# Performance work log

Measured on AMD Instinct MI355X. Metric: run time of the kernel, lower is better.

## Reference

```python
import jax, jax.numpy as jnp
import numpy as np

N = 100000      # nodes
DIN = 64        # input feature dim
H = 64          # hidden dim
OUT = 2         # classifier output dim
E_REL = 1600000 # edges per relation
E_Q = 1000000   # query edges to classify


def _deg_norm(idx, n, dtype):
    # D^{-1/2} with zero-degree -> 0 (DGL norm='both' semantics)
    deg = jax.ops.segment_sum(jnp.ones(idx.shape[0], dtype=dtype), idx, num_segments=n)
    return jnp.where(deg > 0, jax.lax.rsqrt(jnp.maximum(deg, 1.0)), 0.0)


def graph_conv(x, src, dst, W, b):
    # DGL GraphConv, norm='both': out = D_in^{-1/2} A D_out^{-1/2} x W + b
    n = x.shape[0]
    c_src = _deg_norm(src, n, x.dtype)   # out-degree norm on src side
    c_dst = _deg_norm(dst, n, x.dtype)   # in-degree norm on dst side
    h = x * c_src[:, None]
    agg = jax.ops.segment_sum(h[src], dst, num_segments=n)  # gather -> scatter-add
    agg = agg * c_dst[:, None]
    return agg @ W + b


def setup_inputs() -> dict:
    key = jax.random.key(0)
    ks = jax.random.split(key, 16)
    x = jax.random.normal(ks[0], (N, DIN), dtype=jnp.float32)
    src_pos = jax.random.randint(ks[1], (E_REL,), 0, N)
    dst_pos = jax.random.randint(ks[2], (E_REL,), 0, N)
    src_neg = jax.random.randint(ks[3], (E_REL,), 0, N)
    dst_neg = jax.random.randint(ks[4], (E_REL,), 0, N)
    edge_index = jax.random.randint(ks[5], (2, E_Q), 0, N)
    s_in = 1.0 / np.sqrt(DIN)
    s_h = 1.0 / np.sqrt(H)
    return {
        "x": x,
        "W0_pos": jax.random.uniform(ks[6], (DIN, H), jnp.float32, -s_in, s_in),
        "b0_pos": jnp.zeros((H,), jnp.float32),
        "W0_neg": jax.random.uniform(ks[7], (DIN, H), jnp.float32, -s_in, s_in),
        "b0_neg": jnp.zeros((H,), jnp.float32),
        "W1_pos": jax.random.uniform(ks[8], (H, H), jnp.float32, -s_h, s_h),
        "b1_pos": jnp.zeros((H,), jnp.float32),
        "W1_neg": jax.random.uniform(ks[9], (H, H), jnp.float32, -s_h, s_h),
        "b1_neg": jnp.zeros((H,), jnp.float32),
        "Wc": jax.random.uniform(ks[10], (2 * H, OUT), jnp.float32, -s_h, s_h),
        "bc": jnp.zeros((OUT,), jnp.float32),
        "src_pos": src_pos, "dst_pos": dst_pos,
        "src_neg": src_neg, "dst_neg": dst_neg,
        "edge_index": edge_index,
    }


def reference(x, W0_pos, b0_pos, W0_neg, b0_neg, W1_pos, b1_pos, W1_neg, b1_neg,
              Wc, bc, src_pos, dst_pos, src_neg, dst_neg, edge_index):
    # Layer 1: per-relation GraphConv on input feats, ReLU (HeteroGraphConv 'all' keeps per-relation streams)
    h_pos = jax.nn.relu(graph_conv(x, src_pos, dst_pos, W0_pos, b0_pos))
    h_neg = jax.nn.relu(graph_conv(x, src_neg, dst_neg, W0_neg, b0_neg))
    # Layer 2: each relation stream convolved on its own relation graph
    z_pos = jax.nn.relu(graph_conv(h_pos, src_pos, dst_pos, W1_pos, b1_pos))
    z_neg = jax.nn.relu(graph_conv(h_neg, src_neg, dst_neg, W1_neg, b1_neg))
    z = z_pos - z_neg                         # [N, H]
    src_ids, dst_ids = edge_index[0], edge_index[1]
    h_pair = jnp.concatenate([z[src_ids], z[dst_ids]], axis=1)  # [E_Q, 2H]
    logits = h_pair @ Wc + bc
    return z, jax.nn.sigmoid(logits)
```

## Files before the change

kernel.cpp:

```cpp
#include <hip/hip_runtime.h>
#include <hip/hip_fp16.h>
#include <math.h>

#define N_NODES 100000
#define DIM 64
#define E_REL 1600000
#define E_QQ 1000000

#define NBUCK 196
#define BCAP 9216
#define CHUNK_E 8192
#define P1_BLOCKS ((E_REL + CHUNK_E - 1) / CHUNK_E)

__global__ __launch_bounds__(256) void bin_edges(
    const int* __restrict__ src, const int* __restrict__ dst,
    int* __restrict__ gcur_d, int* __restrict__ gcur_s,
    unsigned* __restrict__ bin_d, unsigned* __restrict__ bin_s) {
  __shared__ int cd[NBUCK];
  __shared__ int cs[NBUCK];
  int t = threadIdx.x;
  for (int i = t; i < NBUCK; i += 256) { cd[i] = 0; cs[i] = 0; }
  __syncthreads();
  int e0 = blockIdx.x * CHUNK_E;
  int e1 = e0 + CHUNK_E;
  if (e1 > E_REL) e1 = E_REL;
  for (int e = e0 + t; e < e1; e += 256) {
    atomicAdd(&cd[dst[e] >> 9], 1);
    atomicAdd(&cs[src[e] >> 9], 1);
  }
  __syncthreads();
  for (int i = t; i < NBUCK; i += 256) {
    cd[i] = atomicAdd(&gcur_d[i], cd[i]);
    cs[i] = atomicAdd(&gcur_s[i], cs[i]);
  }
  __syncthreads();
  for (int e = e0 + t; e < e1; e += 256) {
    int s = src[e];
    int d = dst[e];
    int bd = d >> 9;
    int bs = s >> 9;
    int pd = atomicAdd(&cd[bd], 1);
    int ps = atomicAdd(&cs[bs], 1);
    if ((unsigned)pd < BCAP)
      bin_d[(size_t)bd * BCAP + pd] = (unsigned)(((d & 511) << 17) | s);
    if ((unsigned)ps < BCAP)
      bin_s[(size_t)bs * BCAP + ps] = (unsigned)s;
  }
}

__global__ __launch_bounds__(256) void build_tables(
    const unsigned* __restrict__ bin_d, const int* __restrict__ gcur_d,
    const unsigned* __restrict__ bin_s, const int* __restrict__ gcur_s,
    int* __restrict__ offs, int* __restrict__ degv, int* __restrict__ srclist,
    float* __restrict__ csrc) {
  __shared__ int cnt[512];
  __shared__ int off0[512];
  __shared__ int curv[512];
  __shared__ int ls[256];
  int t = threadIdx.x;
  if (blockIdx.x >= NBUCK) {
    int b = blockIdx.x - NBUCK;
    cnt[t] = 0;
    cnt[t + 256] = 0;
    __syncthreads();
    int n = gcur_s[b];
    if (n > BCAP) n = BCAP;
    const unsigned* be = bin_s + (size_t)b * BCAP;
    for (int i = t; i < n; i += 256) atomicAdd(&cnt[be[i] & 511], 1);
    __syncthreads();
    int node0 = b << 9;
    for (int i = t; i < 512; i += 256) {
      int node = node0 + i;
      if (node < N_NODES) {
        int d = cnt[i];
        csrc[node] = d > 0 ? rsqrtf((float)d) : 0.0f;
      }
    }
    return;
  }
  int b = blockIdx.x;
  cnt[t] = 0;
  cnt[t + 256] = 0;
  __syncthreads();
  int n = gcur_d[b];
  if (n > BCAP) n = BCAP;
  const unsigned* be = bin_d + (size_t)b * BCAP;
  for (int i = t; i < n; i += 256) atomicAdd(&cnt[be[i] >> 17], 1);
  __syncthreads();
  int c0 = cnt[2 * t], c1 = cnt[2 * t + 1];
  ls[t] = c0 + c1;
  __syncthreads();
  for (int off = 1; off < 256; off <<= 1) {
    int v = (t >= off) ? ls[t - off] : 0;
    __syncthreads();
    ls[t] += v;
    __syncthreads();
  }
  int base = ls[t] - (c0 + c1);
  off0[2 * t] = base;
  off0[2 * t + 1] = base + c0;
  curv[2 * t] = base;
  curv[2 * t + 1] = base + c0;
  __syncthreads();
  for (int i = t; i < n; i += 256) {
    unsigned p = be[i];
    int dl = p >> 17;
    int pos = atomicAdd(&curv[dl], 1);
    srclist[(size_t)b * BCAP + pos] = (int)(p & 0x1FFFF);
  }
  __syncthreads();
  int node0 = b << 9;
  for (int i = t; i < 512; i += 256) {
    int node = node0 + i;
    if (node < N_NODES) {
      offs[node] = b * BCAP + off0[i];
      degv[node] = cnt[i];
    }
  }
}

__device__ inline unsigned pack_h2(float a, float b) {
  __half2 h = __floats2half2_rn(a, b);
  return *reinterpret_cast<unsigned*>(&h);
}

__global__ __launch_bounds__(256) void gemm_in_h(
    const float* __restrict__ X, const float* __restrict__ W,
    const float* __restrict__ csrc, __half* __restrict__ Y) {
  __shared__ float Ws[64 * 64];
  for (int t = threadIdx.x; t < 64 * 64; t += 256) Ws[t] = W[t];
  __syncthreads();
  int row = blockIdx.x * 256 + threadIdx.x;
  if (row >= N_NODES) return;
  const float4* xr = (const float4*)(X + (size_t)row * 64);
  float acc[64];
#pragma unroll
  for (int j = 0; j < 64; j++) acc[j] = 0.0f;
#pragma unroll
  for (int k4 = 0; k4 < 16; k4++) {
    float4 xv = xr[k4];
    const float* w0 = &Ws[(k4 * 4 + 0) * 64];
    const float* w1 = &Ws[(k4 * 4 + 1) * 64];
    const float* w2 = &Ws[(k4 * 4 + 2) * 64];
    const float* w3 = &Ws[(k4 * 4 + 3) * 64];
#pragma unroll
    for (int j = 0; j < 64; j++)
      acc[j] += xv.x * w0[j] + xv.y * w1[j] + xv.z * w2[j] + xv.w * w3[j];
  }
  float s = csrc[row];
  uint4* yr = (uint4*)(Y + (size_t)row * 64);
#pragma unroll
  for (int j8 = 0; j8 < 8; j8++) {
    uint4 u;
    u.x = pack_h2(s * acc[j8 * 8 + 0], s * acc[j8 * 8 + 1]);
    u.y = pack_h2(s * acc[j8 * 8 + 2], s * acc[j8 * 8 + 3]);
    u.z = pack_h2(s * acc[j8 * 8 + 4], s * acc[j8 * 8 + 5]);
    u.w = pack_h2(s * acc[j8 * 8 + 6], s * acc[j8 * 8 + 7]);
    yr[j8] = u;
  }
}

__device__ inline float4 agg_quad(const __half* __restrict__ Y, int beg,
                                  int deg, const int* __restrict__ srclist,
                                  int lane, int l, int q) {
  float4 a0 = make_float4(0.f, 0.f, 0.f, 0.f);
  float4 a1 = make_float4(0.f, 0.f, 0.f, 0.f);
  const __half* Yl = Y + 4 * l;
  for (int base = 0; base < deg; base += 64) {
    int chunk = deg - base;
    if (chunk > 64) chunk = 64;
    int sv = (base + lane < deg) ? srclist[beg + base + lane] : 0;
    int nq8 = chunk & ~7;
    for (int j = 0; j < nq8; j += 8) {
      int s0 = __shfl(sv, j + q);
      int s1 = __shfl(sv, j + 4 + q);
      uint2 u0 = *(const uint2*)(Yl + (size_t)s0 * 64);
      uint2 u1 = *(const uint2*)(Yl + (size_t)s1 * 64);
      float2 f;
      f = __half22float2(*reinterpret_cast<__half2*>(&u0.x));
      a0.x += f.x; a0.y += f.y;
      f = __half22float2(*reinterpret_cast<__half2*>(&u0.y));
      a0.z += f.x; a0.w += f.y;
      f = __half22float2(*reinterpret_cast<__half2*>(&u1.x));
      a1.x += f.x; a1.y += f.y;
      f = __half22float2(*reinterpret_cast<__half2*>(&u1.y));
      a1.z += f.x; a1.w += f.y;
    }
    int j0 = nq8 + q;
    int j1 = nq8 + 4 + q;
    int s0 = __shfl(sv, j0 & 63);
    int s1 = __shfl(sv, j1 & 63);
    if (j0 < chunk) {
      uint2 u = *(const uint2*)(Yl + (size_t)s0 * 64);
      float2 f;
      f = __half22float2(*reinterpret_cast<__half2*>(&u.x));
      a0.x += f.x; a0.y += f.y;
      f = __half22float2(*reinterpret_cast<__half2*>(&u.y));
      a0.z += f.x; a0.w += f.y;
    }
    if (j1 < chunk) {
      uint2 u = *(const uint2*)(Yl + (size_t)s1 * 64);
      float2 f;
      f = __half22float2(*reinterpret_cast<__half2*>(&u.x));
      a1.x += f.x; a1.y += f.y;
      f = __half22float2(*reinterpret_cast<__half2*>(&u.y));
      a1.z += f.x; a1.w += f.y;
    }
  }
  a0.x += a1.x; a0.y += a1.y; a0.z += a1.z; a0.w += a1.w;
  a0.x += __shfl_xor(a0.x, 16); a0.y += __shfl_xor(a0.y, 16);
  a0.z += __shfl_xor(a0.z, 16); a0.w += __shfl_xor(a0.w, 16);
  a0.x += __shfl_xor(a0.x, 32); a0.y += __shfl_xor(a0.y, 32);
  a0.z += __shfl_xor(a0.z, 32); a0.w += __shfl_xor(a0.w, 32);
  return a0;
}

__global__ __launch_bounds__(256) void gather_mid(
    const __half* __restrict__ Y, const int* __restrict__ offs,
    const int* __restrict__ degv, const int* __restrict__ srclist,
    const float* __restrict__ b0, const float* __restrict__ csrc,
    const float* __restrict__ W1, __half* __restrict__ Y2) {
  __shared__ float Ws[64 * 64];
  __shared__ float hs[4][64];
  for (int t = threadIdx.x; t < 64 * 64; t += 256) Ws[t] = W1[t];
  __syncthreads();
  int wid = (blockIdx.x * 256 + threadIdx.x) >> 6;
  int lane = threadIdx.x & 63;
  int wslot = threadIdx.x >> 6;
  if (wid >= N_NODES) return;
  int l = lane & 15, q = lane >> 4;
  int beg = offs[wid];
  int deg = degv[wid];
  float4 acc = agg_quad(Y, beg, deg, srclist, lane, l, q);
  float cd = deg > 0 ? rsqrtf((float)deg) : 0.0f;
  float4 bv = ((const float4*)b0)[l];
  float4 h;
  h.x = fmaxf(acc.x * cd + bv.x, 0.0f);
  h.y = fmaxf(acc.y * cd + bv.y, 0.0f);
  h.z = fmaxf(acc.z * cd + bv.z, 0.0f);
  h.w = fmaxf(acc.w * cd + bv.w, 0.0f);
  if (lane < 16) *((float4*)&hs[wslot][4 * l]) = h;
  float acc2 = 0.0f;
#pragma unroll
  for (int k4 = 0; k4 < 16; k4++) {
    float4 hv = *((const float4*)&hs[wslot][4 * k4]);
    acc2 += hv.x * Ws[(4 * k4 + 0) * 64 + lane] +
            hv.y * Ws[(4 * k4 + 1) * 64 + lane] +
            hv.z * Ws[(4 * k4 + 2) * 64 + lane] +
            hv.w * Ws[(4 * k4 + 3) * 64 + lane];
  }
  Y2[(size_t)wid * 64 + lane] = __float2half(csrc[wid] * acc2);
}

template <int MODE>
__global__ __launch_bounds__(256) void gather_fin(
    const __half* __restrict__ Y2, const int* __restrict__ offs,
    const int* __restrict__ degv, const int* __restrict__ srclist,
    const float* __restrict__ b1, float* __restrict__ z,
    float* __restrict__ uv, const float* __restrict__ Wc) {
  __shared__ float Wcs[256];
  if (MODE == 1) {
    Wcs[threadIdx.x] = Wc[threadIdx.x];
    __syncthreads();
  }
  int wid = (blockIdx.x * 256 + threadIdx.x) >> 6;
  int lane = threadIdx.x & 63;
  if (wid >= N_NODES) return;
  int l = lane & 15, q = lane >> 4;
  int beg = offs[wid];
  int deg = degv[wid];
  float4 acc = agg_quad(Y2, beg, deg, srclist, lane, l, q);
  float cd = deg > 0 ? rsqrtf((float)deg) : 0.0f;
  float4 bv = ((const float4*)b1)[l];
  float4 v;
  v.x = fmaxf(acc.x * cd + bv.x, 0.0f);
  v.y = fmaxf(acc.y * cd + bv.y, 0.0f);
  v.z = fmaxf(acc.z * cd + bv.z, 0.0f);
  v.w = fmaxf(acc.w * cd + bv.w, 0.0f);
  float* zrow = z + (size_t)wid * 64 + 4 * l;
  if (MODE == 0) {
    if (lane < 16) *((float4*)zrow) = v;
  } else {
    float4 zo = *((const float4*)zrow);
    float4 r;
    r.x = zo.x - v.x; r.y = zo.y - v.y; r.z = zo.z - v.z; r.w = zo.w - v.w;
    if (lane < 16) *((float4*)zrow) = r;
    float pu0 = r.x * Wcs[(4 * l + 0) * 2 + 0] + r.y * Wcs[(4 * l + 1) * 2 + 0] +
                r.z * Wcs[(4 * l + 2) * 2 + 0] + r.w * Wcs[(4 * l + 3) * 2 + 0];
    float pu1 = r.x * Wcs[(4 * l + 0) * 2 + 1] + r.y * Wcs[(4 * l + 1) * 2 + 1] +
                r.z * Wcs[(4 * l + 2) * 2 + 1] + r.w * Wcs[(4 * l + 3) * 2 + 1];
    float pv0 = r.x * Wcs[(64 + 4 * l + 0) * 2 + 0] + r.y * Wcs[(64 + 4 * l + 1) * 2 + 0] +
                r.z * Wcs[(64 + 4 * l + 2) * 2 + 0] + r.w * Wcs[(64 + 4 * l + 3) * 2 + 0];
    float pv1 = r.x * Wcs[(64 + 4 * l + 0) * 2 + 1] + r.y * Wcs[(64 + 4 * l + 1) * 2 + 1] +
                r.z * Wcs[(64 + 4 * l + 2) * 2 + 1] + r.w * Wcs[(64 + 4 * l + 3) * 2 + 1];
#pragma unroll
    for (int o = 1; o < 16; o <<= 1) {
      pu0 += __shfl_xor(pu0, o);
      pu1 += __shfl_xor(pu1, o);
      pv0 += __shfl_xor(pv0, o);
      pv1 += __shfl_xor(pv1, o);
    }
    if (lane == 0) {
      float4 o4 = make_float4(pu0, pu1, pv0, pv1);
      *((float4*)(uv + (size_t)wid * 4)) = o4;
    }
  }
}

__global__ __launch_bounds__(256) void classify_kernel(
    const float* __restrict__ uv, const int* __restrict__ ei,
    const float* __restrict__ bc, float* __restrict__ out) {
  int e = blockIdx.x * 256 + threadIdx.x;
  if (e >= E_QQ) return;
  int s = ei[e];
  int d = ei[E_QQ + e];
  float4 us = *((const float4*)(uv + (size_t)s * 4));
  float4 vd = *((const float4*)(uv + (size_t)d * 4));
  float l0 = us.x + vd.z + bc[0];
  float l1 = us.y + vd.w + bc[1];
  float2 o;
  o.x = 1.0f / (1.0f + __expf(-l0));
  o.y = 1.0f / (1.0f + __expf(-l1));
  *((float2*)(out + (size_t)e * 2)) = o;
}

extern "C" void kernel_launch(void* const* d_in, const int* in_sizes, int n_in,
                              void* d_out, int out_size, void* d_ws,
                              size_t ws_size, hipStream_t stream) {
  const float* x   = (const float*)d_in[0];
  const float* W0p = (const float*)d_in[1];
  const float* b0p = (const float*)d_in[2];
  const float* W0n = (const float*)d_in[3];
  const float* b0n = (const float*)d_in[4];
  const float* W1p = (const float*)d_in[5];
  const float* b1p = (const float*)d_in[6];
  const float* W1n = (const float*)d_in[7];
  const float* b1n = (const float*)d_in[8];
  const float* Wc  = (const float*)d_in[9];
  const float* bc  = (const float*)d_in[10];
  const int* sp = (const int*)d_in[11];
  const int* dp = (const int*)d_in[12];
  const int* sn = (const int*)d_in[13];
  const int* dn = (const int*)d_in[14];
  const int* ei = (const int*)d_in[15];

  float* csrc_p = (float*)d_ws;
  float* csrc_n = csrc_p + N_NODES;
  int* offs_p = (int*)(csrc_n + N_NODES);
  int* deg_p  = offs_p + N_NODES;
  int* offs_n = deg_p + N_NODES;
  int* deg_n  = offs_n + N_NODES;
  float* uv   = (float*)(deg_n + N_NODES);
  int* gcur   = (int*)(uv + 4 * N_NODES);
  unsigned* bin_d = (unsigned*)(gcur + 2 * NBUCK + 2);
  unsigned* bin_s = bin_d + (size_t)NBUCK * BCAP;
  int* srclist = (int*)(bin_s + (size_t)NBUCK * BCAP);
  __half* A = (__half*)(srclist + (size_t)NBUCK * BCAP);
  __half* B = A + (size_t)N_NODES * 64;

  float* z     = (float*)d_out;
  float* probs = z + (size_t)N_NODES * 64;

  int* gcur_d = gcur;
  int* gcur_s = gcur + NBUCK;

  const int gemmGrid = (N_NODES + 255) / 256;
  const int aggGrid  = (N_NODES * 64 + 255) / 256;

  hipMemsetAsync(gcur, 0, 2 * NBUCK * sizeof(int), stream);
  bin_edges<<<P1_BLOCKS, 256, 0, stream>>>(sp, dp, gcur_d, gcur_s, bin_d, bin_s);
  build_tables<<<2 * NBUCK, 256, 0, stream>>>(bin_d, gcur_d, bin_s, gcur_s,
                                              offs_p, deg_p, srclist, csrc_p);
  gemm_in_h<<<gemmGrid, 256, 0, stream>>>(x, W0p, csrc_p, A);
  gather_mid<<<aggGrid, 256, 0, stream>>>(A, offs_p, deg_p, srclist, b0p,
                                          csrc_p, W1p, B);
  gather_fin<0><<<aggGrid, 256, 0, stream>>>(B, offs_p, deg_p, srclist, b1p, z,
                                             uv, Wc);

  hipMemsetAsync(gcur, 0, 2 * NBUCK * sizeof(int), stream);
  bin_edges<<<P1_BLOCKS, 256, 0, stream>>>(sn, dn, gcur_d, gcur_s, bin_d, bin_s);
  build_tables<<<2 * NBUCK, 256, 0, stream>>>(bin_d, gcur_d, bin_s, gcur_s,
                                              offs_n, deg_n, srclist, csrc_n);
  gemm_in_h<<<gemmGrid, 256, 0, stream>>>(x, W0n, csrc_n, A);
  gather_mid<<<aggGrid, 256, 0, stream>>>(A, offs_n, deg_n, srclist, b0n,
                                          csrc_n, W1n, B);
  gather_fin<1><<<aggGrid, 256, 0, stream>>>(B, offs_n, deg_n, srclist, b1n, z,
                                             uv, Wc);

  classify_kernel<<<(E_QQ + 255) / 256, 256, 0, stream>>>(uv, ei, bc, probs);
}
```

Baseline: 629.1 us.

## Drop src binning for global atomic degrees, persist gather kernels, widen unroll

Out-degree is now counted with global atomics into a per-node array, so the source-side bin pass and its bin_s buffer go away. build_tables now runs 1024-thread blocks over the dst buckets only and writes csrc from the atomic counts. The gather kernels become grid-stride loops over a fixed 2048 blocks so the W1 load into shared memory is paid once per block, and W1 is stored transposed with an XOR swizzle for float4 reads. The neighbor loop is unrolled to 16 with fdot2-based half accumulation, and the edge chunk size is reduced. The global atomics may contend on popular nodes, and there are several independent changes at once.

```diff
diff --git a/kernel.cpp b/kernel.cpp
--- a/kernel.cpp
+++ b/kernel.cpp
@@ -9,113 +9,86 @@
 
 #define NBUCK 196
 #define BCAP 9216
-#define CHUNK_E 8192
+#define CHUNK_E 2048
 #define P1_BLOCKS ((E_REL + CHUNK_E - 1) / CHUNK_E)
+#define AGG_BLOCKS 2048
+#define AGG_STRIDE (AGG_BLOCKS * 4)
 
 __global__ __launch_bounds__(256) void bin_edges(
     const int* __restrict__ src, const int* __restrict__ dst,
-    int* __restrict__ gcur_d, int* __restrict__ gcur_s,
-    unsigned* __restrict__ bin_d, unsigned* __restrict__ bin_s) {
+    int* __restrict__ gcur_d, int* __restrict__ odeg,
+    unsigned* __restrict__ bin_d) {
   __shared__ int cd[NBUCK];
-  __shared__ int cs[NBUCK];
   int t = threadIdx.x;
-  for (int i = t; i < NBUCK; i += 256) { cd[i] = 0; cs[i] = 0; }
+  for (int i = t; i < NBUCK; i += 256) cd[i] = 0;
   __syncthreads();
   int e0 = blockIdx.x * CHUNK_E;
   int e1 = e0 + CHUNK_E;
   if (e1 > E_REL) e1 = E_REL;
   for (int e = e0 + t; e < e1; e += 256) {
     atomicAdd(&cd[dst[e] >> 9], 1);
-    atomicAdd(&cs[src[e] >> 9], 1);
+    atomicAdd(&odeg[src[e]], 1);
   }
   __syncthreads();
   for (int i = t; i < NBUCK; i += 256) {
-    cd[i] = atomicAdd(&gcur_d[i], cd[i]);
-    cs[i] = atomicAdd(&gcur_s[i], cs[i]);
+    int c = cd[i];
+    cd[i] = c > 0 ? atomicAdd(&gcur_d[i], c) : 0;
   }
   __syncthreads();
   for (int e = e0 + t; e < e1; e += 256) {
     int s = src[e];
     int d = dst[e];
     int bd = d >> 9;
-    int bs = s >> 9;
     int pd = atomicAdd(&cd[bd], 1);
-    int ps = atomicAdd(&cs[bs], 1);
     if ((unsigned)pd < BCAP)
       bin_d[(size_t)bd * BCAP + pd] = (unsigned)(((d & 511) << 17) | s);
-    if ((unsigned)ps < BCAP)
-      bin_s[(size_t)bs * BCAP + ps] = (unsigned)s;
-  }
-}
-
-__global__ __launch_bounds__(256) void build_tables(
+  }
+}
+
+__global__ __launch_bounds__(1024) void build_tables(
     const unsigned* __restrict__ bin_d, const int* __restrict__ gcur_d,
-    const unsigned* __restrict__ bin_s, const int* __restrict__ gcur_s,
-    int* __restrict__ offs, int* __restrict__ degv, int* __restrict__ srclist,
+    const int* __restrict__ odeg, int* __restrict__ offs,
+    int* __restrict__ degv, int* __restrict__ srclist,
     float* __restrict__ csrc) {
   __shared__ int cnt[512];
   __shared__ int off0[512];
   __shared__ int curv[512];
-  __shared__ int ls[256];
+  __shared__ int ls[512];
   int t = threadIdx.x;
-  if (blockIdx.x >= NBUCK) {
-    int b = blockIdx.x - NBUCK;
-    cnt[t] = 0;
-    cnt[t + 256] = 0;
-    __syncthreads();
-    int n = gcur_s[b];
-    if (n > BCAP) n = BCAP;
-    const unsigned* be = bin_s + (size_t)b * BCAP;
-    for (int i = t; i < n; i += 256) atomicAdd(&cnt[be[i] & 511], 1);
-    __syncthreads();
-    int node0 = b << 9;
-    for (int i = t; i < 512; i += 256) {
-      int node = node0 + i;
-      if (node < N_NODES) {
-        int d = cnt[i];
-        csrc[node] = d > 0 ? rsqrtf((float)d) : 0.0f;
-      }
-    }
-    return;
-  }
   int b = blockIdx.x;
-  cnt[t] = 0;
-  cnt[t + 256] = 0;
+  if (t < 512) cnt[t] = 0;
   __syncthreads();
   int n = gcur_d[b];
   if (n > BCAP) n = BCAP;
   const unsigned* be = bin_d + (size_t)b * BCAP;
-  for (int i = t; i < n; i += 256) atomicAdd(&cnt[be[i] >> 17], 1);
-  __syncthreads();
-  int c0 = cnt[2 * t], c1 = cnt[2 * t + 1];
-  ls[t] = c0 + c1;
-  __syncthreads();
-  for (int off = 1; off < 256; off <<= 1) {
-    int v = (t >= off) ? ls[t - off] : 0;
+  for (int i = t; i < n; i += 1024) atomicAdd(&cnt[be[i] >> 17], 1);
+  __syncthreads();
+  if (t < 512) ls[t] = cnt[t];
+  __syncthreads();
+  for (int off = 1; off < 512; off <<= 1) {
+    int v = 0;
+    if (t < 512 && t >= off) v = ls[t - off];
     __syncthreads();
-    ls[t] += v;
+    if (t < 512) ls[t] += v;
     __syncthreads();
   }
-  int base = ls[t] - (c0 + c1);
-  off0[2 * t] = base;
-  off0[2 * t + 1] = base + c0;
-  curv[2 * t] = base;
-  curv[2 * t + 1] = base + c0;
-  __syncthreads();
-  for (int i = t; i < n; i += 256) {
+  if (t < 512) {
+    int base = ls[t] - cnt[t];
+    off0[t] = base;
+    curv[t] = base;
+  }
+  __syncthreads();
+  for (int i = t; i < n; i += 1024) {
     unsigned p = be[i];
-    int dl = p >> 17;
-    int pos = atomicAdd(&curv[dl], 1);
+    int pos = atomicAdd(&curv[p >> 17], 1);
     srclist[(size_t)b * BCAP + pos] = (int)(p & 0x1FFFF);
   }
-  __syncthreads();
-  int node0 = b << 9;
-  for (int i = t; i < 512; i += 256) {
-    int node = node0 + i;
-    if (node < N_NODES) {
-      offs[node] = b * BCAP + off0[i];
-      degv[node] = cnt[i];
-    }
+  int node = (b << 9) + t;
+  if (t < 512 && node < N_NODES) {
+    offs[node] = b * BCAP + off0[t];
+    degv[node] = cnt[t];
+    int od = odeg[node];
+    csrc[node] = od > 0 ? rsqrtf((float)od) : 0.0f;
   }
 }
 
@@ -158,6 +131,16 @@
     u.w = pack_h2(s * acc[j8 * 8 + 6], s * acc[j8 * 8 + 7]);
     yr[j8] = u;
   }
+}
+
+typedef _Float16 half2r __attribute__((ext_vector_type(2)));
+
+__device__ inline void dacc(unsigned w, float& a, float& b) {
+  half2r v = __builtin_bit_cast(half2r, w);
+  const half2r m10 = {(_Float16)1.0f, (_Float16)0.0f};
+  const half2r m01 = {(_Float16)0.0f, (_Float16)1.0f};
+  a = __builtin_amdgcn_fdot2(v, m10, a, false);
+  b = __builtin_amdgcn_fdot2(v, m01, b, false);
 }
 
 __device__ inline float4 agg_quad(const __half* __restrict__ Y, int beg,
@@ -170,41 +153,31 @@
     int chunk = deg - base;
     if (chunk > 64) chunk = 64;
     int sv = (base + lane < deg) ? srclist[beg + base + lane] : 0;
-    int nq8 = chunk & ~7;
-    for (int j = 0; j < nq8; j += 8) {
+    int nq16 = chunk & ~15;
+    for (int j = 0; j < nq16; j += 16) {
       int s0 = __shfl(sv, j + q);
       int s1 = __shfl(sv, j + 4 + q);
+      int s2 = __shfl(sv, j + 8 + q);
+      int s3 = __shfl(sv, j + 12 + q);
       uint2 u0 = *(const uint2*)(Yl + (size_t)s0 * 64);
       uint2 u1 = *(const uint2*)(Yl + (size_t)s1 * 64);
-      float2 f;
-      f = __half22float2(*reinterpret_cast<__half2*>(&u0.x));
-      a0.x += f.x; a0.y += f.y;
-      f = __half22float2(*reinterpret_cast<__half2*>(&u0.y));
-      a0.z += f.x; a0.w += f.y;
-      f = __half22float2(*reinterpret_cast<__half2*>(&u1.x));
-      a1.x += f.x; a1.y += f.y;
-      f = __half22float2(*reinterpret_cast<__half2*>(&u1.y));
-      a1.z += f.x; a1.w += f.y;
+      uint2 u2 = *(const uint2*)(Yl + (size_t)s2 * 64);
+      uint2 u3 = *(const uint2*)(Yl + (size_t)s3 * 64);
+      dacc(u0.x, a0.x, a0.y); dacc(u0.y, a0.z, a0.w);
+      dacc(u1.x, a1.x, a1.y); dacc(u1.y, a1.z, a1.w);
+      dacc(u2.x, a0.x, a0.y); dacc(u2.y, a0.z, a0.w);
+      dacc(u3.x, a1.x, a1.y); dacc(u3.y, a1.z, a1.w);
     }
-    int j0 = nq8 + q;
-    int j1 = nq8 + 4 + q;
-    int s0 = __shfl(sv, j0 & 63);
-    int s1 = __shfl(sv, j1 & 63);
-    if (j0 < chunk) {
-      uint2 u = *(const uint2*)(Yl + (size_t)s0 * 64);
-      float2 f;
-      f = __half22float2(*reinterpret_cast<__half2*>(&u.x));
-      a0.x += f.x; a0.y += f.y;
-      f = __half22float2(*reinterpret_cast<__half2*>(&u.y));
-      a0.z += f.x; a0.w += f.y;
-    }
-    if (j1 < chunk) {
-      uint2 u = *(const uint2*)(Yl + (size_t)s1 * 64);
-      float2 f;
-      f = __half22float2(*reinterpret_cast<__half2*>(&u.x));
-      a1.x += f.x; a1.y += f.y;
-      f = __half22float2(*reinterpret_cast<__half2*>(&u.y));
-      a1.z += f.x; a1.w += f.y;
+    int jt = nq16 + q;
+#pragma unroll
+    for (int ts = 0; ts < 4; ts++) {
+      int jj = jt + 4 * ts;
+      int s = __shfl(sv, jj & 63);
+      if (jj < chunk) {
+        uint2 u = *(const uint2*)(Yl + (size_t)s * 64);
+        if (ts & 1) { dacc(u.x, a1.x, a1.y); dacc(u.y, a1.z, a1.w); }
+        else        { dacc(u.x, a0.x, a0.y); dacc(u.y, a0.z, a0.w); }
+      }
     }
   }
   a0.x += a1.x; a0.y += a1.y; a0.z += a1.z; a0.w += a1.w;
@@ -220,36 +193,38 @@
     const int* __restrict__ degv, const int* __restrict__ srclist,
     const float* __restrict__ b0, const float* __restrict__ csrc,
     const float* __restrict__ W1, __half* __restrict__ Y2) {
-  __shared__ float Ws[64 * 64];
+  __shared__ float WsT[64 * 64];
   __shared__ float hs[4][64];
-  for (int t = threadIdx.x; t < 64 * 64; t += 256) Ws[t] = W1[t];
-  __syncthreads();
-  int wid = (blockIdx.x * 256 + threadIdx.x) >> 6;
+  for (int i = threadIdx.x; i < 64 * 64; i += 256) {
+    int k = i >> 6, o = i & 63;
+    int c = (k >> 2) ^ (o & 7);
+    WsT[o * 64 + (c << 2) + (k & 3)] = W1[i];
+  }
+  __syncthreads();
   int lane = threadIdx.x & 63;
   int wslot = threadIdx.x >> 6;
-  if (wid >= N_NODES) return;
   int l = lane & 15, q = lane >> 4;
-  int beg = offs[wid];
-  int deg = degv[wid];
-  float4 acc = agg_quad(Y, beg, deg, srclist, lane, l, q);
-  float cd = deg > 0 ? rsqrtf((float)deg) : 0.0f;
   float4 bv = ((const float4*)b0)[l];
-  float4 h;
-  h.x = fmaxf(acc.x * cd + bv.x, 0.0f);
-  h.y = fmaxf(acc.y * cd + bv.y, 0.0f);
-  h.z = fmaxf(acc.z * cd + bv.z, 0.0f);
-  h.w = fmaxf(acc.w * cd + bv.w, 0.0f);
-  if (lane < 16) *((float4*)&hs[wslot][4 * l]) = h;
-  float acc2 = 0.0f;
-#pragma unroll
-  for (int k4 = 0; k4 < 16; k4++) {
-    float4 hv = *((const float4*)&hs[wslot][4 * k4]);
-    acc2 += hv.x * Ws[(4 * k4 + 0) * 64 + lane] +
-            hv.y * Ws[(4 * k4 + 1) * 64 + lane] +
-            hv.z * Ws[(4 * k4 + 2) * 64 + lane] +
-            hv.w * Ws[(4 * k4 + 3) * 64 + lane];
-  }
-  Y2[(size_t)wid * 64 + lane] = __float2half(csrc[wid] * acc2);
+  for (int wid = blockIdx.x * 4 + wslot; wid < N_NODES; wid += AGG_STRIDE) {
+    int beg = offs[wid];
+    int deg = degv[wid];
+    float4 acc = agg_quad(Y, beg, deg, srclist, lane, l, q);
+    float cd = deg > 0 ? rsqrtf((float)deg) : 0.0f;
+    float4 h;
+    h.x = fmaxf(acc.x * cd + bv.x, 0.0f);
+    h.y = fmaxf(acc.y * cd + bv.y, 0.0f);
+    h.z = fmaxf(acc.z * cd + bv.z, 0.0f);
+    h.w = fmaxf(acc.w * cd + bv.w, 0.0f);
+    if (lane < 16) *((float4*)&hs[wslot][4 * l]) = h;
+    float acc2 = 0.0f;
+#pragma unroll
+    for (int k4 = 0; k4 < 16; k4++) {
+      float4 hv = *((const float4*)&hs[wslot][4 * k4]);
+      float4 w = *((const float4*)&WsT[lane * 64 + ((k4 ^ (lane & 7)) << 2)]);
+      acc2 += hv.x * w.x + hv.y * w.y + hv.z * w.z + hv.w * w.w;
+    }
+    Y2[(size_t)wid * 64 + lane] = __float2half(csrc[wid] * acc2);
+  }
 }
 
 template <int MODE>
@@ -263,46 +238,47 @@
     Wcs[threadIdx.x] = Wc[threadIdx.x];
     __syncthreads();
   }
-  int wid = (blockIdx.x * 256 + threadIdx.x) >> 6;
   int lane = threadIdx.x & 63;
-  if (wid >= N_NODES) return;
+  int wslot = threadIdx.x >> 6;
   int l = lane & 15, q = lane >> 4;
-  int beg = offs[wid];
-  int deg = degv[wid];
-  float4 acc = agg_quad(Y2, beg, deg, srclist, lane, l, q);
-  float cd = deg > 0 ? rsqrtf((float)deg) : 0.0f;
   float4 bv = ((const float4*)b1)[l];
-  float4 v;
-  v.x = fmaxf(acc.x * cd + bv.x, 0.0f);
-  v.y = fmaxf(acc.y * cd + bv.y, 0.0f);
-  v.z = fmaxf(acc.z * cd + bv.z, 0.0f);
-  v.w = fmaxf(acc.w * cd + bv.w, 0.0f);
-  float* zrow = z + (size_t)wid * 64 + 4 * l;
-  if (MODE == 0) {
-    if (lane < 16) *((float4*)zrow) = v;
-  } else {
-    float4 zo = *((const float4*)zrow);
-    float4 r;
-    r.x = zo.x - v.x; r.y = zo.y - v.y; r.z = zo.z - v.z; r.w = zo.w - v.w;
-    if (lane < 16) *((float4*)zrow) = r;
-    float pu0 = r.x * Wcs[(4 * l + 0) * 2 + 0] + r.y * Wcs[(4 * l + 1) * 2 + 0] +
-                r.z * Wcs[(4 * l + 2) * 2 + 0] + r.w * Wcs[(4 * l + 3) * 2 + 0];
-    float pu1 = r.x * Wcs[(4 * l + 0) * 2 + 1] + r.y * Wcs[(4 * l + 1) * 2 + 1] +
-                r.z * Wcs[(4 * l + 2) * 2 + 1] + r.w * Wcs[(4 * l + 3) * 2 + 1];
-    float pv0 = r.x * Wcs[(64 + 4 * l + 0) * 2 + 0] + r.y * Wcs[(64 + 4 * l + 1) * 2 + 0] +
-                r.z * Wcs[(64 + 4 * l + 2) * 2 + 0] + r.w * Wcs[(64 + 4 * l + 3) * 2 + 0];
-    float pv1 = r.x * Wcs[(64 + 4 * l + 0) * 2 + 1] + r.y * Wcs[(64 + 4 * l + 1) * 2 + 1] +
-                r.z * Wcs[(64 + 4 * l + 2) * 2 + 1] + r.w * Wcs[(64 + 4 * l + 3) * 2 + 1];
-#pragma unroll
-    for (int o = 1; o < 16; o <<= 1) {
-      pu0 += __shfl_xor(pu0, o);
-      pu1 += __shfl_xor(pu1, o);
-      pv0 += __shfl_xor(pv0, o);
-      pv1 += __shfl_xor(pv1, o);
-    }
-    if (lane == 0) {
-      float4 o4 = make_float4(pu0, pu1, pv0, pv1);
-      *((float4*)(uv + (size_t)wid * 4)) = o4;
+  for (int wid = blockIdx.x * 4 + wslot; wid < N_NODES; wid += AGG_STRIDE) {
+    int beg = offs[wid];
+    int deg = degv[wid];
+    float4 acc = agg_quad(Y2, beg, deg, srclist, lane, l, q);
+    float cd = deg > 0 ? rsqrtf((float)deg) : 0.0f;
+    float4 v;
+    v.x = fmaxf(acc.x * cd + bv.x, 0.0f);
+    v.y = fmaxf(acc.y * cd + bv.y, 0.0f);
+    v.z = fmaxf(acc.z * cd + bv.z, 0.0f);
+    v.w = fmaxf(acc.w * cd + bv.w, 0.0f);
+    float* zrow = z + (size_t)wid * 64 + 4 * l;
+    if (MODE == 0) {
+      if (lane < 16) *((float4*)zrow) = v;
+    } else {
+      float4 zo = *((const float4*)zrow);
+      float4 r;
+      r.x = zo.x - v.x; r.y = zo.y - v.y; r.z = zo.z - v.z; r.w = zo.w - v.w;
+      if (lane < 16) *((float4*)zrow) = r;
+      float pu0 = r.x * Wcs[(4 * l + 0) * 2 + 0] + r.y * Wcs[(4 * l + 1) * 2 + 0] +
+                  r.z * Wcs[(4 * l + 2) * 2 + 0] + r.w * Wcs[(4 * l + 3) * 2 + 0];
+      float pu1 = r.x * Wcs[(4 * l + 0) * 2 + 1] + r.y * Wcs[(4 * l + 1) * 2 + 1] +
+                  r.z * Wcs[(4 * l + 2) * 2 + 1] + r.w * Wcs[(4 * l + 3) * 2 + 1];
+      float pv0 = r.x * Wcs[(64 + 4 * l + 0) * 2 + 0] + r.y * Wcs[(64 + 4 * l + 1) * 2 + 0] +
+                  r.z * Wcs[(64 + 4 * l + 2) * 2 + 0] + r.w * Wcs[(64 + 4 * l + 3) * 2 + 0];
+      float pv1 = r.x * Wcs[(64 + 4 * l + 0) * 2 + 1] + r.y * Wcs[(64 + 4 * l + 1) * 2 + 1] +
+                  r.z * Wcs[(64 + 4 * l + 2) * 2 + 1] + r.w * Wcs[(64 + 4 * l + 3) * 2 + 1];
+#pragma unroll
+      for (int o = 1; o < 16; o <<= 1) {
+        pu0 += __shfl_xor(pu0, o);
+        pu1 += __shfl_xor(pu1, o);
+        pv0 += __shfl_xor(pv0, o);
+        pv1 += __shfl_xor(pv1, o);
+      }
+      if (lane == 0) {
+        float4 o4 = make_float4(pu0, pu1, pv0, pv1);
+        *((float4*)(uv + (size_t)wid * 4)) = o4;
+      }
     }
   }
 }
@@ -351,41 +327,37 @@
   int* offs_n = deg_p + N_NODES;
   int* deg_n  = offs_n + N_NODES;
   float* uv   = (float*)(deg_n + N_NODES);
-  int* gcur   = (int*)(uv + 4 * N_NODES);
-  unsigned* bin_d = (unsigned*)(gcur + 2 * NBUCK + 2);
-  unsigned* bin_s = bin_d + (size_t)NBUCK * BCAP;
-  int* srclist = (int*)(bin_s + (size_t)NBUCK * BCAP);
+  int* odeg   = (int*)(uv + 4 * N_NODES);
+  int* gcur   = odeg + N_NODES;
+  unsigned* bin_d = (unsigned*)(gcur + NBUCK + 4);
+  int* srclist = (int*)(bin_d + (size_t)NBUCK * BCAP);
   __half* A = (__half*)(srclist + (size_t)NBUCK * BCAP);
   __half* B = A + (size_t)N_NODES * 64;
 
   float* z     = (float*)d_out;
   float* probs = z + (size_t)N_NODES * 64;
 
-  int* gcur_d = gcur;
-  int* gcur_s = gcur + NBUCK;
-
   const int gemmGrid = (N_NODES + 255) / 256;
-  const int aggGrid  = (N_NODES * 64 + 255) / 256;
-
-  hipMemsetAsync(gcur, 0, 2 * NBUCK * sizeof(int), stream);
-  bin_edges<<<P1_BLOCKS, 256, 0, stream>>>(sp, dp, gcur_d, gcur_s, bin_d, bin_s);
-  build_tables<<<2 * NBUCK, 256, 0, stream>>>(bin_d, gcur_d, bin_s, gcur_s,
-                                              offs_p, deg_p, srclist, csrc_p);
+
+  hipMemsetAsync(odeg, 0, (N_NODES + NBUCK + 4) * sizeof(int), stream);
+  bin_edges<<<P1_BLOCKS, 256, 0, stream>>>(sp, dp, gcur, odeg, bin_d);
+  build_tables<<<NBUCK, 1024, 0, stream>>>(bin_d, gcur, odeg, offs_p, deg_p,
+                                           srclist, csrc_p);
   gemm_in_h<<<gemmGrid, 256, 0, stream>>>(x, W0p, csrc_p, A);
-  gather_mid<<<aggGrid, 256, 0, stream>>>(A, offs_p, deg_p, srclist, b0p,
-                                          csrc_p, W1p, B);
-  gather_fin<0><<<aggGrid, 256, 0, stream>>>(B, offs_p, deg_p, srclist, b1p, z,
-                                             uv, Wc);
-
-  hipMemsetAsync(gcur, 0, 2 * NBUCK * sizeof(int), stream);
-  bin_edges<<<P1_BLOCKS, 256, 0, stream>>>(sn, dn, gcur_d, gcur_s, bin_d, bin_s);
-  build_tables<<<2 * NBUCK, 256, 0, stream>>>(bin_d, gcur_d, bin_s, gcur_s,
-                                              offs_n, deg_n, srclist, csrc_n);
+  gather_mid<<<AGG_BLOCKS, 256, 0, stream>>>(A, offs_p, deg_p, srclist, b0p,
+                                             csrc_p, W1p, B);
+  gather_fin<0><<<AGG_BLOCKS, 256, 0, stream>>>(B, offs_p, deg_p, srclist, b1p,
+                                                z, uv, Wc);
+
+  hipMemsetAsync(odeg, 0, (N_NODES + NBUCK + 4) * sizeof(int), stream);
+  bin_edges<<<P1_BLOCKS, 256, 0, stream>>>(sn, dn, gcur, odeg, bin_d);
+  build_tables<<<NBUCK, 1024, 0, stream>>>(bin_d, gcur, odeg, offs_n, deg_n,
+                                           srclist, csrc_n);
   gemm_in_h<<<gemmGrid, 256, 0, stream>>>(x, W0n, csrc_n, A);
-  gather_mid<<<aggGrid, 256, 0, stream>>>(A, offs_n, deg_n, srclist, b0n,
-                                          csrc_n, W1n, B);
-  gather_fin<1><<<aggGrid, 256, 0, stream>>>(B, offs_n, deg_n, srclist, b1n, z,
-                                             uv, Wc);
+  gather_mid<<<AGG_BLOCKS, 256, 0, stream>>>(A, offs_n, deg_n, srclist, b0n,
+                                             csrc_n, W1n, B);
+  gather_fin<1><<<AGG_BLOCKS, 256, 0, stream>>>(B, offs_n, deg_n, srclist, b1n,
+                                                z, uv, Wc);
 
   classify_kernel<<<(E_QQ + 255) / 256, 256, 0, stream>>>(uv, ei, bc, probs);
 }
```

New measurement: 683.7 us. +8.7%, slower.

## Vectorize edge binning, unroll gather with fdot2, persistent aggregation blocks

Applied to the files above, without the earlier changes.

Edge binning now processes int4-vectorized loads with a smaller chunk size and skips global atomics for empty buckets. The neighbor-gather inner loop is unrolled to four outstanding row loads and accumulates half pairs via the fdot2 builtin instead of explicit half-to-float conversion. Aggregation kernels become grid-stride persistent loops over 2048 blocks, amortizing weight staging to shared memory, and the W1 shared copy is transposed with an XOR swizzle so each lane reads float4 rows without bank conflicts. The int4 path assumes CHUNK_E divisible by 4 and aligned inputs, and the persistent launch may reduce latency hiding if occupancy drops.

```diff
diff --git a/kernel.cpp b/kernel.cpp
--- a/kernel.cpp
+++ b/kernel.cpp
@@ -9,8 +9,10 @@
 
 #define NBUCK 196
 #define BCAP 9216
-#define CHUNK_E 8192
+#define CHUNK_E 4096
 #define P1_BLOCKS ((E_REL + CHUNK_E - 1) / CHUNK_E)
+#define AGG_BLOCKS 2048
+#define AGG_STRIDE (AGG_BLOCKS * 4)
 
 __global__ __launch_bounds__(256) void bin_edges(
     const int* __restrict__ src, const int* __restrict__ dst,
@@ -22,29 +24,47 @@
   for (int i = t; i < NBUCK; i += 256) { cd[i] = 0; cs[i] = 0; }
   __syncthreads();
   int e0 = blockIdx.x * CHUNK_E;
-  int e1 = e0 + CHUNK_E;
-  if (e1 > E_REL) e1 = E_REL;
-  for (int e = e0 + t; e < e1; e += 256) {
-    atomicAdd(&cd[dst[e] >> 9], 1);
-    atomicAdd(&cs[src[e] >> 9], 1);
+  int n = E_REL - e0;
+  if (n > CHUNK_E) n = CHUNK_E;
+  int n4 = n >> 2;
+  const int4* s4 = (const int4*)(src + e0);
+  const int4* d4 = (const int4*)(dst + e0);
+  for (int i = t; i < n4; i += 256) {
+    int4 dv = d4[i];
+    atomicAdd(&cd[dv.x >> 9], 1);
+    atomicAdd(&cd[dv.y >> 9], 1);
+    atomicAdd(&cd[dv.z >> 9], 1);
+    atomicAdd(&cd[dv.w >> 9], 1);
+    int4 sv = s4[i];
+    atomicAdd(&cs[sv.x >> 9], 1);
+    atomicAdd(&cs[sv.y >> 9], 1);
+    atomicAdd(&cs[sv.z >> 9], 1);
+    atomicAdd(&cs[sv.w >> 9], 1);
   }
   __syncthreads();
   for (int i = t; i < NBUCK; i += 256) {
-    cd[i] = atomicAdd(&gcur_d[i], cd[i]);
-    cs[i] = atomicAdd(&gcur_s[i], cs[i]);
-  }
-  __syncthreads();
-  for (int e = e0 + t; e < e1; e += 256) {
-    int s = src[e];
-    int d = dst[e];
-    int bd = d >> 9;
-    int bs = s >> 9;
-    int pd = atomicAdd(&cd[bd], 1);
-    int ps = atomicAdd(&cs[bs], 1);
-    if ((unsigned)pd < BCAP)
-      bin_d[(size_t)bd * BCAP + pd] = (unsigned)(((d & 511) << 17) | s);
-    if ((unsigned)ps < BCAP)
-      bin_s[(size_t)bs * BCAP + ps] = (unsigned)s;
+    int c = cd[i];
+    cd[i] = c > 0 ? atomicAdd(&gcur_d[i], c) : 0;
+    c = cs[i];
+    cs[i] = c > 0 ? atomicAdd(&gcur_s[i], c) : 0;
+  }
+  __syncthreads();
+  for (int i = t; i < n4; i += 256) {
+    int4 sv = s4[i];
+    int4 dv = d4[i];
+#pragma unroll
+    for (int k = 0; k < 4; k++) {
+      int s = (&sv.x)[k];
+      int d = (&dv.x)[k];
+      int bd = d >> 9;
+      int bs = s >> 9;
+      int pd = atomicAdd(&cd[bd], 1);
+      int ps = atomicAdd(&cs[bs], 1);
+      if ((unsigned)pd < BCAP)
+        bin_d[(size_t)bd * BCAP + pd] = (unsigned)(((d & 511) << 17) | s);
+      if ((unsigned)ps < BCAP)
+        bin_s[(size_t)bs * BCAP + ps] = (unsigned)s;
+    }
   }
 }
 
@@ -160,6 +180,16 @@
   }
 }
 
+typedef _Float16 half2r __attribute__((ext_vector_type(2)));
+
+__device__ inline void dacc(unsigned w, float& a, float& b) {
+  half2r v = __builtin_bit_cast(half2r, w);
+  const half2r m10 = {(_Float16)1.0f, (_Float16)0.0f};
+  const half2r m01 = {(_Float16)0.0f, (_Float16)1.0f};
+  a = __builtin_amdgcn_fdot2(v, m10, a, false);
+  b = __builtin_amdgcn_fdot2(v, m01, b, false);
+}
+
 __device__ inline float4 agg_quad(const __half* __restrict__ Y, int beg,
                                   int deg, const int* __restrict__ srclist,
                                   int lane, int l, int q) {
@@ -170,41 +200,31 @@
     int chunk = deg - base;
     if (chunk > 64) chunk = 64;
     int sv = (base + lane < deg) ? srclist[beg + base + lane] : 0;
-    int nq8 = chunk & ~7;
-    for (int j = 0; j < nq8; j += 8) {
+    int nq16 = chunk & ~15;
+    for (int j = 0; j < nq16; j += 16) {
       int s0 = __shfl(sv, j + q);
       int s1 = __shfl(sv, j + 4 + q);
+      int s2 = __shfl(sv, j + 8 + q);
+      int s3 = __shfl(sv, j + 12 + q);
       uint2 u0 = *(const uint2*)(Yl + (size_t)s0 * 64);
       uint2 u1 = *(const uint2*)(Yl + (size_t)s1 * 64);
-      float2 f;
-      f = __half22float2(*reinterpret_cast<__half2*>(&u0.x));
-      a0.x += f.x; a0.y += f.y;
-      f = __half22float2(*reinterpret_cast<__half2*>(&u0.y));
-      a0.z += f.x; a0.w += f.y;
-      f = __half22float2(*reinterpret_cast<__half2*>(&u1.x));
-      a1.x += f.x; a1.y += f.y;
-      f = __half22float2(*reinterpret_cast<__half2*>(&u1.y));
-      a1.z += f.x; a1.w += f.y;
-    }
-    int j0 = nq8 + q;
-    int j1 = nq8 + 4 + q;
-    int s0 = __shfl(sv, j0 & 63);
-    int s1 = __shfl(sv, j1 & 63);
-    if (j0 < chunk) {
-      uint2 u = *(const uint2*)(Yl + (size_t)s0 * 64);
-      float2 f;
-      f = __half22float2(*reinterpret_cast<__half2*>(&u.x));
-      a0.x += f.x; a0.y += f.y;
-      f = __half22float2(*reinterpret_cast<__half2*>(&u.y));
-      a0.z += f.x; a0.w += f.y;
-    }
-    if (j1 < chunk) {
-      uint2 u = *(const uint2*)(Yl + (size_t)s1 * 64);
-      float2 f;
-      f = __half22float2(*reinterpret_cast<__half2*>(&u.x));
-      a1.x += f.x; a1.y += f.y;
-      f = __half22float2(*reinterpret_cast<__half2*>(&u.y));
-      a1.z += f.x; a1.w += f.y;
+      uint2 u2 = *(const uint2*)(Yl + (size_t)s2 * 64);
+      uint2 u3 = *(const uint2*)(Yl + (size_t)s3 * 64);
+      dacc(u0.x, a0.x, a0.y); dacc(u0.y, a0.z, a0.w);
+      dacc(u1.x, a1.x, a1.y); dacc(u1.y, a1.z, a1.w);
+      dacc(u2.x, a0.x, a0.y); dacc(u2.y, a0.z, a0.w);
+      dacc(u3.x, a1.x, a1.y); dacc(u3.y, a1.z, a1.w);
+    }
+    int jt = nq16 + q;
+#pragma unroll
+    for (int ts = 0; ts < 4; ts++) {
+      int jj = jt + 4 * ts;
+      int s = __shfl(sv, jj & 63);
+      if (jj < chunk) {
+        uint2 u = *(const uint2*)(Yl + (size_t)s * 64);
+        if (ts & 1) { dacc(u.x, a1.x, a1.y); dacc(u.y, a1.z, a1.w); }
+        else        { dacc(u.x, a0.x, a0.y); dacc(u.y, a0.z, a0.w); }
+      }
     }
   }
   a0.x += a1.x; a0.y += a1.y; a0.z += a1.z; a0.w += a1.w;
@@ -220,36 +240,38 @@
     const int* __restrict__ degv, const int* __restrict__ srclist,
     const float* __restrict__ b0, const float* __restrict__ csrc,
     const float* __restrict__ W1, __half* __restrict__ Y2) {
-  __shared__ float Ws[64 * 64];
+  __shared__ float WsT[64 * 64];
   __shared__ float hs[4][64];
-  for (int t = threadIdx.x; t < 64 * 64; t += 256) Ws[t] = W1[t];
-  __syncthreads();
-  int wid = (blockIdx.x * 256 + threadIdx.x) >> 6;
+  for (int i = threadIdx.x; i < 64 * 64; i += 256) {
+    int k = i >> 6, o = i & 63;
+    int c = (k >> 2) ^ (o & 7);
+    WsT[o * 64 + (c << 2) + (k & 3)] = W1[i];
+  }
+  __syncthreads();
   int lane = threadIdx.x & 63;
   int wslot = threadIdx.x >> 6;
-  if (wid >= N_NODES) return;
   int l = lane & 15, q = lane >> 4;
-  int beg = offs[wid];
-  int deg = degv[wid];
-  float4 acc = agg_quad(Y, beg, deg, srclist, lane, l, q);
-  float cd = deg > 0 ? rsqrtf((float)deg) : 0.0f;
   float4 bv = ((const float4*)b0)[l];
-  float4 h;
-  h.x = fmaxf(acc.x * cd + bv.x, 0.0f);
-  h.y = fmaxf(acc.y * cd + bv.y, 0.0f);
-  h.z = fmaxf(acc.z * cd + bv.z, 0.0f);
-  h.w = fmaxf(acc.w * cd + bv.w, 0.0f);
-  if (lane < 16) *((float4*)&hs[wslot][4 * l]) = h;
-  float acc2 = 0.0f;
-#pragma unroll
-  for (int k4 = 0; k4 < 16; k4++) {
-    float4 hv = *((const float4*)&hs[wslot][4 * k4]);
-    acc2 += hv.x * Ws[(4 * k4 + 0) * 64 + lane] +
-            hv.y * Ws[(4 * k4 + 1) * 64 + lane] +
-            hv.z * Ws[(4 * k4 + 2) * 64 + lane] +
-            hv.w * Ws[(4 * k4 + 3) * 64 + lane];
-  }
-  Y2[(size_t)wid * 64 + lane] = __float2half(csrc[wid] * acc2);
+  for (int wid = blockIdx.x * 4 + wslot; wid < N_NODES; wid += AGG_STRIDE) {
+    int beg = offs[wid];
+    int deg = degv[wid];
+    float4 acc = agg_quad(Y, beg, deg, srclist, lane, l, q);
+    float cd = deg > 0 ? rsqrtf((float)deg) : 0.0f;
+    float4 h;
+    h.x = fmaxf(acc.x * cd + bv.x, 0.0f);
+    h.y = fmaxf(acc.y * cd + bv.y, 0.0f);
+    h.z = fmaxf(acc.z * cd + bv.z, 0.0f);
+    h.w = fmaxf(acc.w * cd + bv.w, 0.0f);
+    if (lane < 16) *((float4*)&hs[wslot][4 * l]) = h;
+    float acc2 = 0.0f;
+#pragma unroll
+    for (int k4 = 0; k4 < 16; k4++) {
+      float4 hv = *((const float4*)&hs[wslot][4 * k4]);
+      float4 w = *((const float4*)&WsT[lane * 64 + ((k4 ^ (lane & 7)) << 2)]);
+      acc2 += hv.x * w.x + hv.y * w.y + hv.z * w.z + hv.w * w.w;
+    }
+    Y2[(size_t)wid * 64 + lane] = __float2half(csrc[wid] * acc2);
+  }
 }
 
 template <int MODE>
@@ -263,46 +285,47 @@
     Wcs[threadIdx.x] = Wc[threadIdx.x];
     __syncthreads();
   }
-  int wid = (blockIdx.x * 256 + threadIdx.x) >> 6;
   int lane = threadIdx.x & 63;
-  if (wid >= N_NODES) return;
+  int wslot = threadIdx.x >> 6;
   int l = lane & 15, q = lane >> 4;
-  int beg = offs[wid];
-  int deg = degv[wid];
-  float4 acc = agg_quad(Y2, beg, deg, srclist, lane, l, q);
-  float cd = deg > 0 ? rsqrtf((float)deg) : 0.0f;
   float4 bv = ((const float4*)b1)[l];
-  float4 v;
-  v.x = fmaxf(acc.x * cd + bv.x, 0.0f);
-  v.y = fmaxf(acc.y * cd + bv.y, 0.0f);
-  v.z = fmaxf(acc.z * cd + bv.z, 0.0f);
-  v.w = fmaxf(acc.w * cd + bv.w, 0.0f);
-  float* zrow = z + (size_t)wid * 64 + 4 * l;
-  if (MODE == 0) {
-    if (lane < 16) *((float4*)zrow) = v;
-  } else {
-    float4 zo = *((const float4*)zrow);
-    float4 r;
-    r.x = zo.x - v.x; r.y = zo.y - v.y; r.z = zo.z - v.z; r.w = zo.w - v.w;
-    if (lane < 16) *((float4*)zrow) = r;
-    float pu0 = r.x * Wcs[(4 * l + 0) * 2 + 0] + r.y * Wcs[(4 * l + 1) * 2 + 0] +
-                r.z * Wcs[(4 * l + 2) * 2 + 0] + r.w * Wcs[(4 * l + 3) * 2 + 0];
-    float pu1 = r.x * Wcs[(4 * l + 0) * 2 + 1] + r.y * Wcs[(4 * l + 1) * 2 + 1] +
-                r.z * Wcs[(4 * l + 2) * 2 + 1] + r.w * Wcs[(4 * l + 3) * 2 + 1];
-    float pv0 = r.x * Wcs[(64 + 4 * l + 0) * 2 + 0] + r.y * Wcs[(64 + 4 * l + 1) * 2 + 0] +
-                r.z * Wcs[(64 + 4 * l + 2) * 2 + 0] + r.w * Wcs[(64 + 4 * l + 3) * 2 + 0];
-    float pv1 = r.x * Wcs[(64 + 4 * l + 0) * 2 + 1] + r.y * Wcs[(64 + 4 * l + 1) * 2 + 1] +
-                r.z * Wcs[(64 + 4 * l + 2) * 2 + 1] + r.w * Wcs[(64 + 4 * l + 3) * 2 + 1];
-#pragma unroll
-    for (int o = 1; o < 16; o <<= 1) {
-      pu0 += __shfl_xor(pu0, o);
-      pu1 += __shfl_xor(pu1, o);
-      pv0 += __shfl_xor(pv0, o);
-      pv1 += __shfl_xor(pv1, o);
-    }
-    if (lane == 0) {
-      float4 o4 = make_float4(pu0, pu1, pv0, pv1);
-      *((float4*)(uv + (size_t)wid * 4)) = o4;
+  for (int wid = blockIdx.x * 4 + wslot; wid < N_NODES; wid += AGG_STRIDE) {
+    int beg = offs[wid];
+    int deg = degv[wid];
+    float4 acc = agg_quad(Y2, beg, deg, srclist, lane, l, q);
+    float cd = deg > 0 ? rsqrtf((float)deg) : 0.0f;
+    float4 v;
+    v.x = fmaxf(acc.x * cd + bv.x, 0.0f);
+    v.y = fmaxf(acc.y * cd + bv.y, 0.0f);
+    v.z = fmaxf(acc.z * cd + bv.z, 0.0f);
+    v.w = fmaxf(acc.w * cd + bv.w, 0.0f);
+    float* zrow = z + (size_t)wid * 64 + 4 * l;
+    if (MODE == 0) {
+      if (lane < 16) *((float4*)zrow) = v;
+    } else {
+      float4 zo = *((const float4*)zrow);
+      float4 r;
+      r.x = zo.x - v.x; r.y = zo.y - v.y; r.z = zo.z - v.z; r.w = zo.w - v.w;
+      if (lane < 16) *((float4*)zrow) = r;
+      float pu0 = r.x * Wcs[(4 * l + 0) * 2 + 0] + r.y * Wcs[(4 * l + 1) * 2 + 0] +
+                  r.z * Wcs[(4 * l + 2) * 2 + 0] + r.w * Wcs[(4 * l + 3) * 2 + 0];
+      float pu1 = r.x * Wcs[(4 * l + 0) * 2 + 1] + r.y * Wcs[(4 * l + 1) * 2 + 1] +
+                  r.z * Wcs[(4 * l + 2) * 2 + 1] + r.w * Wcs[(4 * l + 3) * 2 + 1];
+      float pv0 = r.x * Wcs[(64 + 4 * l + 0) * 2 + 0] + r.y * Wcs[(64 + 4 * l + 1) * 2 + 0] +
+                  r.z * Wcs[(64 + 4 * l + 2) * 2 + 0] + r.w * Wcs[(64 + 4 * l + 3) * 2 + 0];
+      float pv1 = r.x * Wcs[(64 + 4 * l + 0) * 2 + 1] + r.y * Wcs[(64 + 4 * l + 1) * 2 + 1] +
+                  r.z * Wcs[(64 + 4 * l + 2) * 2 + 1] + r.w * Wcs[(64 + 4 * l + 3) * 2 + 1];
+#pragma unroll
+      for (int o = 1; o < 16; o <<= 1) {
+        pu0 += __shfl_xor(pu0, o);
+        pu1 += __shfl_xor(pu1, o);
+        pv0 += __shfl_xor(pv0, o);
+        pv1 += __shfl_xor(pv1, o);
+      }
+      if (lane == 0) {
+        float4 o4 = make_float4(pu0, pu1, pv0, pv1);
+        *((float4*)(uv + (size_t)wid * 4)) = o4;
+      }
     }
   }
 }
@@ -365,27 +388,26 @@
   int* gcur_s = gcur + NBUCK;
 
   const int gemmGrid = (N_NODES + 255) / 256;
-  const int aggGrid  = (N_NODES * 64 + 255) / 256;
 
   hipMemsetAsync(gcur, 0, 2 * NBUCK * sizeof(int), stream);
   bin_edges<<<P1_BLOCKS, 256, 0, stream>>>(sp, dp, gcur_d, gcur_s, bin_d, bin_s);
   build_tables<<<2 * NBUCK, 256, 0, stream>>>(bin_d, gcur_d, bin_s, gcur_s,
                                               offs_p, deg_p, srclist, csrc_p);
   gemm_in_h<<<gemmGrid, 256, 0, stream>>>(x, W0p, csrc_p, A);
-  gather_mid<<<aggGrid, 256, 0, stream>>>(A, offs_p, deg_p, srclist, b0p,
-                                          csrc_p, W1p, B);
-  gather_fin<0><<<aggGrid, 256, 0, stream>>>(B, offs_p, deg_p, srclist, b1p, z,
-                                             uv, Wc);
+  gather_mid<<<AGG_BLOCKS, 256, 0, stream>>>(A, offs_p, deg_p, srclist, b0p,
+                                             csrc_p, W1p, B);
+  gather_fin<0><<<AGG_BLOCKS, 256, 0, stream>>>(B, offs_p, deg_p, srclist, b1p,
+                                                z, uv, Wc);
 
   hipMemsetAsync(gcur, 0, 2 * NBUCK * sizeof(int), stream);
   bin_edges<<<P1_BLOCKS, 256, 0, stream>>>(sn, dn, gcur_d, gcur_s, bin_d, bin_s);
   build_tables<<<2 * NBUCK, 256, 0, stream>>>(bin_d, gcur_d, bin_s, gcur_s,
                                               offs_n, deg_n, srclist, csrc_n);
   gemm_in_h<<<gemmGrid, 256, 0, stream>>>(x, W0n, csrc_n, A);
-  gather_mid<<<aggGrid, 256, 0, stream>>>(A, offs_n, deg_n, srclist, b0n,
-                                          csrc_n, W1n, B);
-  gather_fin<1><<<aggGrid, 256, 0, stream>>>(B, offs_n, deg_n, srclist, b1n, z,
-                                             uv, Wc);
+  gather_mid<<<AGG_BLOCKS, 256, 0, stream>>>(A, offs_n, deg_n, srclist, b0n,
+                                             csrc_n, W1n, B);
+  gather_fin<1><<<AGG_BLOCKS, 256, 0, stream>>>(B, offs_n, deg_n, srclist, b1n,
+                                                z, uv, Wc);
 
   classify_kernel<<<(E_QQ + 255) / 256, 256, 0, stream>>>(uv, ei, bc, probs);
 }
```

Measured after the change: 589.0 us. -6.4%, faster.
